# Kernel optimization log

Hardware: AMD Instinct MI355X
Metric: run time of the kernel (lower is better)

## Reference

```python
import jax, jax.numpy as jnp
import numpy as np

D = 1024
H = 16
DK = D // H


def apply_rope(x):
    # x: [B, H, T, dk]; interleaved-pair RoPE as in the torch source
    T, dim = x.shape[-2], x.shape[-1]
    inv_freq = 1.0 / (10000.0 ** (jnp.arange(0, dim, 2, dtype=x.dtype) / dim))  # [dk/2]
    pos = jnp.arange(T, dtype=x.dtype)
    sinusoid = pos[:, None] * inv_freq[None, :]  # [T, dk/2]
    sin, cos = jnp.sin(sinusoid), jnp.cos(sinusoid)
    x1, x2 = x[..., ::2], x[..., 1::2]
    rot = jnp.stack([x1 * cos - x2 * sin, x1 * sin + x2 * cos], axis=-1)
    return rot.reshape(x.shape)


def setup_inputs() -> dict:
    key = jax.random.key(0)
    k1, k2, k3, k4, k5 = jax.random.split(key, 5)
    B, T = 2, 2048
    s = 1.0 / np.sqrt(D)
    return {
        "x": jax.random.normal(k1, (B, T, D), dtype=jnp.float32),
        "W_qkv": jax.random.normal(k2, (D, 3 * D), dtype=jnp.float32) * s,
        "b_qkv": jnp.zeros((3 * D,), dtype=jnp.float32),
        "W_out": jax.random.normal(k3, (D, D), dtype=jnp.float32) * s,
        "b_out": jnp.zeros((D,), dtype=jnp.float32),
    }


def reference(x, W_qkv, b_qkv, W_out, b_out):
    B, T, C = x.shape
    qkv = x @ W_qkv + b_qkv  # [B, T, 3D]
    qkv = qkv.reshape(B, T, 3, H, DK).transpose(2, 0, 3, 1, 4)  # [3, B, H, T, dk]
    q, k, v = qkv[0], qkv[1], qkv[2]
    q, k = apply_rope(q), apply_rope(k)
    scores = jnp.einsum("bhtd,bhsd->bhts", q, k) / jnp.sqrt(jnp.asarray(DK, x.dtype))
    causal = jnp.tril(jnp.ones((T, T), dtype=bool))
    scores = jnp.where(causal, scores, jnp.asarray(-1e9, x.dtype))
    probs = jax.nn.softmax(scores, axis=-1)
    attn = jnp.einsum("bhts,bhsd->bhtd", probs, v)  # [B, H, T, dk]
    out = attn.transpose(0, 2, 1, 3).reshape(B, T, C)  # b h t d -> b t (h d)
    return out @ W_out + b_out
```

## Files before the change

### kernel.cpp

```cpp
#include <hip/hip_runtime.h>
#include <math.h>

#define DMODEL 1024
#define NHEAD  16
#define HDK    64
#define BATCH  2
#define SEQ    2048
#define MROWS  (BATCH*SEQ)
#define NQKV   (3*DMODEL)
#define LOG2_10000 13.287712379549449f
#define INV2PI 0.15915494309189535f
#define SCALE_LOG2E 0.1803368801111137f
#define M_FIX 8.0f

typedef __attribute__((ext_vector_type(8))) short bf16x8;
typedef __attribute__((ext_vector_type(4))) short s16x4;
typedef __attribute__((ext_vector_type(4))) float f32x4;
typedef __attribute__((ext_vector_type(2))) unsigned int u32x2;

__device__ __forceinline__ short f2bf(float f) {
    union { float f; unsigned u; } v; v.f = f;
    unsigned r = v.u + 0x7fffu + ((v.u >> 16) & 1u);
    return (short)(r >> 16);
}

__device__ __forceinline__ float fast_exp2(float x) {
#if __has_builtin(__builtin_amdgcn_exp2f)
    return __builtin_amdgcn_exp2f(x);
#else
    return exp2f(x);
#endif
}

__device__ __forceinline__ void gld_lds16(const short* g, short* l) {
    __builtin_amdgcn_global_load_lds(
        (const __attribute__((address_space(1))) void*)g,
        (__attribute__((address_space(3))) void*)l, 16, 0, 0);
}

__global__ __launch_bounds__(256) void prep_kernel(
    const float* __restrict__ x, const float* __restrict__ wqkv,
    const float* __restrict__ wout,
    short* __restrict__ xb, short* __restrict__ wqkv_t, short* __restrict__ wout_t)
{
    __shared__ short tile[32][33];
    const int tid = threadIdx.x;
    if (blockIdx.x < 2048) {
        const int i = (blockIdx.x * 256 + tid) * 8;
        float4 a = *(const float4*)(x + i);
        float4 b = *(const float4*)(x + i + 4);
        bf16x8 o;
        o[0] = f2bf(a.x); o[1] = f2bf(a.y); o[2] = f2bf(a.z); o[3] = f2bf(a.w);
        o[4] = f2bf(b.x); o[5] = f2bf(b.y); o[6] = f2bf(b.z); o[7] = f2bf(b.w);
        *(bf16x8*)(xb + i) = o;
        return;
    }
    const int bx = blockIdx.x - 2048;
    int nx = bx & 127;
    const int ky = bx >> 7;
    const float* in; short* out; int N;
    if (nx < 96) { in = wqkv; out = wqkv_t; N = NQKV; }
    else         { in = wout; out = wout_t; N = DMODEL; nx -= 96; }
    const int tx = tid & 31, ty = tid >> 5;
    const int n0 = nx * 32, k0 = ky * 32;
    #pragma unroll
    for (int i = 0; i < 32; i += 8)
        tile[ty + i][tx] = f2bf(in[(size_t)(k0 + ty + i) * N + n0 + tx]);
    __syncthreads();
    #pragma unroll
    for (int i = 0; i < 32; i += 8)
        out[(size_t)(n0 + ty + i) * DMODEL + k0 + tx] = tile[tx][ty + i];
}

__global__ __launch_bounds__(256) void qkv_gemm_kernel(
    const short* __restrict__ xb, const short* __restrict__ Wt,
    const float* __restrict__ bias,
    short* __restrict__ qd, short* __restrict__ kd, short* __restrict__ vtb)
{
    __shared__ __align__(16) short As[3][128 * 32];
    __shared__ __align__(16) short Bs[3][128 * 32];
    const int tid = threadIdx.x;
    const int lane = tid & 63, wave = tid >> 6;
    const int wm = wave & 1, wn = wave >> 1;
    const int l15 = lane & 15, quad = lane >> 4;
    const int n0 = blockIdx.x * 128, m0 = blockIdx.y * 128;
    const int srow = lane >> 2, sc = lane & 3;
    const int scp = sc ^ ((srow >> 1) & 3);
    const int rdx = (l15 >> 1) & 3;

    const short* gA1 = xb + (size_t)(m0 + wave * 32 + srow) * DMODEL + scp * 8;
    const short* gA2 = gA1 + (size_t)16 * DMODEL;
    const short* gB1 = Wt + (size_t)(n0 + wave * 32 + srow) * DMODEL + scp * 8;
    const short* gB2 = gB1 + (size_t)16 * DMODEL;
    const int lofsA1 = (wave * 32) * 32;
    const int lofsA2 = (wave * 32 + 16) * 32;

    f32x4 zero = {0.f, 0.f, 0.f, 0.f};
    f32x4 acc[4][4];
    #pragma unroll
    for (int i = 0; i < 4; ++i)
        #pragma unroll
        for (int j = 0; j < 4; ++j) acc[i][j] = zero;

#define QKV_COMPUTE(CUR)                                                          \
    {                                                                             \
        bf16x8 af[4], bfr[4];                                                     \
        _Pragma("unroll")                                                         \
        for (int i = 0; i < 4; ++i)                                               \
            af[i] = *(const bf16x8*)&As[CUR][(wm * 64 + i * 16 + l15) * 32 + (quad ^ rdx) * 8]; \
        _Pragma("unroll")                                                         \
        for (int j = 0; j < 4; ++j)                                               \
            bfr[j] = *(const bf16x8*)&Bs[CUR][(wn * 64 + j * 16 + l15) * 32 + (quad ^ rdx) * 8]; \
        _Pragma("unroll")                                                         \
        for (int i = 0; i < 4; ++i)                                               \
            _Pragma("unroll")                                                     \
            for (int j = 0; j < 4; ++j)                                           \
                acc[i][j] = __builtin_amdgcn_mfma_f32_16x16x32_bf16(af[i], bfr[j], acc[i][j], 0, 0, 0); \
    }

    gld_lds16(gA1, &As[0][lofsA1]);
    gld_lds16(gA2, &As[0][lofsA2]);
    gld_lds16(gB1, &Bs[0][lofsA1]);
    gld_lds16(gB2, &Bs[0][lofsA2]);
    gld_lds16(gA1 + 32, &As[1][lofsA1]);
    gld_lds16(gA2 + 32, &As[1][lofsA2]);
    gld_lds16(gB1 + 32, &Bs[1][lofsA1]);
    gld_lds16(gB2 + 32, &Bs[1][lofsA2]);

    int cur = 0, nx = 2;
    #pragma unroll 3
    for (int k = 0; k < 30; ++k) {
        const int kn = (k + 2) * 32;
        gld_lds16(gA1 + kn, &As[nx][lofsA1]);
        gld_lds16(gA2 + kn, &As[nx][lofsA2]);
        gld_lds16(gB1 + kn, &Bs[nx][lofsA1]);
        gld_lds16(gB2 + kn, &Bs[nx][lofsA2]);
        asm volatile("s_waitcnt vmcnt(8)\n\ts_barrier" ::: "memory");
        QKV_COMPUTE(cur);
        asm volatile("s_barrier" ::: "memory");
        cur = (cur == 2) ? 0 : cur + 1;
        nx  = (nx == 2) ? 0 : nx + 1;
    }
    asm volatile("s_waitcnt vmcnt(4)\n\ts_barrier" ::: "memory");
    QKV_COMPUTE(cur);
    cur = (cur == 2) ? 0 : cur + 1;
    asm volatile("s_waitcnt vmcnt(0)\n\ts_barrier" ::: "memory");
    QKV_COMPUTE(cur);
#undef QKV_COMPUTE

    const int which = n0 >> 10;
    float biasv[4], invf[4];
    int hh[4], dd[4];
    #pragma unroll
    for (int j = 0; j < 4; ++j) {
        const int n = n0 + wn * 64 + j * 16 + l15;
        biasv[j] = bias[n];
        hh[j] = (n & 1023) >> 6;
        dd[j] = n & 63;
        invf[j] = INV2PI * exp2f(-((float)(dd[j] & ~1) / 64.f) * LOG2_10000);
    }
    #pragma unroll
    for (int i = 0; i < 4; ++i) {
        const int mb = m0 + wm * 64 + i * 16 + quad * 4;
        const int b = mb >> 11, tb = mb & (SEQ - 1);
        if (which < 2) {
            #pragma unroll
            for (int j = 0; j < 4; ++j) {
                #pragma unroll
                for (int r = 0; r < 4; ++r) {
                    const int t = tb + r;
                    float val = acc[i][j][r] + biasv[j];
                    const float rev = (float)t * invf[j];
                    const float fr = rev - floorf(rev);
                    const float s = __builtin_amdgcn_sinf(fr);
                    const float c = __builtin_amdgcn_cosf(fr);
                    const float partner = __shfl_xor(val, 1);
                    val = (lane & 1) ? (partner * s + val * c) : (val * c - partner * s);
                    short* dst = (which == 0) ? qd : kd;
                    dst[((size_t)(b * NHEAD + hh[j]) * SEQ + t) * HDK + dd[j]] = f2bf(val);
                }
            }
        } else {
            #pragma unroll
            for (int j = 0; j < 4; ++j) {
                s16x4 sv;
                #pragma unroll
                for (int r = 0; r < 4; ++r)
                    sv[r] = f2bf(acc[i][j][r] + biasv[j]);
                *(s16x4*)&vtb[((size_t)(b * NHEAD + hh[j]) * HDK + dd[j]) * SEQ + tb] = sv;
            }
        }
    }
}

__global__ __launch_bounds__(512) void attn_mfma_kernel(
    const short* __restrict__ qd, const short* __restrict__ kd,
    const short* __restrict__ vt, short* __restrict__ od)
{
    __shared__ __align__(16) short Ks[2][2][64 * 32];
    __shared__ __align__(16) short Vs[2][2][64 * 32];
    __shared__ __align__(16) short Ps[8][16 * 64];
    const int tid = threadIdx.x, lane = tid & 63, w = tid >> 6;
    const int l15 = lane & 15, quad = lane >> 4;
    const int par = w >> 2;
    const int ws = w & 3;
    const int id = (int)blockIdx.x;
    const int c = id & 7, g = id >> 3;
    const int qt = 31 - (g >> 2);
    const int jj = g & 3;
    const int hb = c + 8 * jj;
    const int h = hb & 15, b = hb >> 4;
    const size_t base = ((size_t)(b * NHEAD + h)) * SEQ * HDK;
    const int stid = tid & 255;
    const int hi = tid >> 8;
    const int srow = stid >> 2, sc = stid & 3;
    const int lofs = srow * 32 + (sc ^ ((srow >> 1) & 3)) * 8;
    const int rdx = (l15 >> 1) & 3;
    const int pmask = (l15 & 3) << 2;
    f32x4 zero = {0.f, 0.f, 0.f, 0.f};

    const short* kp = kd + base + (size_t)(hi * 64 + srow) * HDK + sc * 8;
    const short* vp = vt + base + (size_t)srow * SEQ + hi * 64 + sc * 8;

    const int q0 = qt * 64;
    const int trow = q0 + ws * 16 + l15;
    bf16x8 qf[2];
    {
        const short* qrow = qd + base + (size_t)trow * HDK;
        qf[0] = *(const bf16x8*)(qrow + quad * 8);
        qf[1] = *(const bf16x8*)(qrow + 32 + quad * 8);
    }
    float l_acc = 0.f;
    f32x4 o[4];
    #pragma unroll
    for (int j = 0; j < 4; ++j) o[j] = zero;

    const int nkt = qt + 1;
    const int npair = (nkt + 1) >> 1;
    short* myPs = &Ps[w][0];

    bf16x8 rk[2], rv[2];
    rk[0] = *(const bf16x8*)kp; rk[1] = *(const bf16x8*)(kp + 32);
    rv[0] = *(const bf16x8*)vp; rv[1] = *(const bf16x8*)(vp + 32);

    for (int p = 0; p < npair; ++p) {
        __syncthreads();
        *(bf16x8*)&Ks[hi][0][lofs] = rk[0];
        *(bf16x8*)&Ks[hi][1][lofs] = rk[1];
        *(bf16x8*)&Vs[hi][0][lofs] = rv[0];
        *(bf16x8*)&Vs[hi][1][lofs] = rv[1];
        __syncthreads();
        if (p + 1 < npair) {
            const int sn = (2 * p + 2) * 64;
            const short* kn = kp + (size_t)sn * HDK;
            const short* vn = vp + sn;
            rk[0] = *(const bf16x8*)kn; rk[1] = *(const bf16x8*)(kn + 32);
            rv[0] = *(const bf16x8*)vn; rv[1] = *(const bf16x8*)(vn + 32);
        }

        const int kt = 2 * p + par;
        if (kt < nkt) {
            f32x4 sacc[4];
            __builtin_amdgcn_s_setprio(1);
            #pragma unroll
            for (int j = 0; j < 4; ++j) {
                const int ro = (j * 16 + l15) * 32 + (quad ^ rdx) * 8;
                bf16x8 kf0 = *(const bf16x8*)&Ks[par][0][ro];
                bf16x8 kf1 = *(const bf16x8*)&Ks[par][1][ro];
                sacc[j] = __builtin_amdgcn_mfma_f32_16x16x32_bf16(kf0, qf[0], zero, 0, 0, 0);
                sacc[j] = __builtin_amdgcn_mfma_f32_16x16x32_bf16(kf1, qf[1], sacc[j], 0, 0, 0);
            }
            __builtin_amdgcn_s_setprio(0);
            if (kt == nkt - 1) {
                const int s0 = kt * 64;
                #pragma unroll
                for (int j = 0; j < 4; ++j) {
                    float pv[4];
                    #pragma unroll
                    for (int r = 0; r < 4; ++r) {
                        const int scol = s0 + j * 16 + quad * 4 + r;
                        const float sv = sacc[j][r] * SCALE_LOG2E - M_FIX;
                        pv[r] = (scol > trow) ? 0.f : fast_exp2(sv);
                        l_acc += pv[r];
                    }
                    unsigned pk0, pk1;
                    asm("v_cvt_pk_bf16_f32 %0, %1, %2" : "=v"(pk0) : "v"(pv[0]), "v"(pv[1]));
                    asm("v_cvt_pk_bf16_f32 %0, %1, %2" : "=v"(pk1) : "v"(pv[2]), "v"(pv[3]));
                    const int cc = (j * 4 + quad) ^ pmask;
                    u32x2 pkv = {pk0, pk1};
                    *(u32x2*)&myPs[l15 * 64 + cc * 4] = pkv;
                }
            } else {
                #pragma unroll
                for (int j = 0; j < 4; ++j) {
                    float pv[4];
                    #pragma unroll
                    for (int r = 0; r < 4; ++r) {
                        pv[r] = fast_exp2(sacc[j][r] * SCALE_LOG2E - M_FIX);
                        l_acc += pv[r];
                    }
                    unsigned pk0, pk1;
                    asm("v_cvt_pk_bf16_f32 %0, %1, %2" : "=v"(pk0) : "v"(pv[0]), "v"(pv[1]));
                    asm("v_cvt_pk_bf16_f32 %0, %1, %2" : "=v"(pk1) : "v"(pv[2]), "v"(pv[3]));
                    const int cc = (j * 4 + quad) ^ pmask;
                    u32x2 pkv = {pk0, pk1};
                    *(u32x2*)&myPs[l15 * 64 + cc * 4] = pkv;
                }
            }
            bf16x8 pf0 = *(const bf16x8*)&myPs[l15 * 64 + ((quad * 2) ^ pmask) * 4];
            bf16x8 pf1 = *(const bf16x8*)&myPs[l15 * 64 + ((8 + quad * 2) ^ pmask) * 4];
            __builtin_amdgcn_s_setprio(1);
            #pragma unroll
            for (int j = 0; j < 4; ++j) {
                const int ro = (j * 16 + l15) * 32 + (quad ^ rdx) * 8;
                bf16x8 vf0 = *(const bf16x8*)&Vs[par][0][ro];
                bf16x8 vf1 = *(const bf16x8*)&Vs[par][1][ro];
                o[j] = __builtin_amdgcn_mfma_f32_16x16x32_bf16(pf0, vf0, o[j], 0, 0, 0);
                o[j] = __builtin_amdgcn_mfma_f32_16x16x32_bf16(pf1, vf1, o[j], 0, 0, 0);
            }
            __builtin_amdgcn_s_setprio(0);
        }
    }

    float sr = l_acc;
    sr += __shfl_xor(sr, 16);
    sr += __shfl_xor(sr, 32);

    __syncthreads();
    float* ob   = (float*)&Ks[0][0][0];
    float* lbuf = (float*)&Vs[0][0][0];
    lbuf[w * 16 + l15] = sr;
    if (par == 1) {
        const int bi = (ws * 64 + lane) * 16;
        #pragma unroll
        for (int j = 0; j < 4; ++j)
            #pragma unroll
            for (int r = 0; r < 4; ++r) ob[bi + j * 4 + r] = o[j][r];
    }
    __syncthreads();
    if (par == 0) {
        const int bi = (ws * 64 + lane) * 16;
        #pragma unroll
        for (int j = 0; j < 4; ++j)
            #pragma unroll
            for (int r = 0; r < 4; ++r) o[j][r] += ob[bi + j * 4 + r];

        #pragma unroll
        for (int r = 0; r < 4; ++r) {
            const int qq = quad * 4 + r;
            const float lt = lbuf[ws * 16 + qq] + lbuf[(ws + 4) * 16 + qq];
            const float inv = 1.f / lt;
            const int t = q0 + ws * 16 + qq;
            #pragma unroll
            for (int j = 0; j < 4; ++j)
                od[((size_t)(b * SEQ + t) * NHEAD + h) * HDK + j * 16 + l15] =
                    f2bf(o[j][r] * inv);
        }
    }
}

__global__ __launch_bounds__(256) void out_gemm_kernel(
    const short* __restrict__ Ab, const short* __restrict__ Wt,
    const float* __restrict__ bias, float* __restrict__ out)
{
    __shared__ __align__(16) short As[2][128 * 32];
    __shared__ __align__(16) short Bs[2][64 * 32];
    const int tid = threadIdx.x;
    const int lane = tid & 63, wave = tid >> 6;
    const int wm = wave & 1, wn = wave >> 1;
    const int l15 = lane & 15, quad = lane >> 4;
    const int n0 = blockIdx.x * 64, m0 = blockIdx.y * 128;
    const int srow = lane >> 2, sc = lane & 3;
    const int scp = sc ^ ((srow >> 1) & 3);
    const int rdx = (l15 >> 1) & 3;

    const short* gA1 = Ab + (size_t)(m0 + wave * 32 + srow) * DMODEL + scp * 8;
    const short* gA2 = gA1 + (size_t)16 * DMODEL;
    const short* gB1 = Wt + (size_t)(n0 + wave * 16 + srow) * DMODEL + scp * 8;
    const int lofsA1 = (wave * 32) * 32;
    const int lofsA2 = (wave * 32 + 16) * 32;
    const int lofsB  = (wave * 16) * 32;

    f32x4 zero = {0.f, 0.f, 0.f, 0.f};
    f32x4 acc[4][2];
    #pragma unroll
    for (int i = 0; i < 4; ++i)
        #pragma unroll
        for (int j = 0; j < 2; ++j) acc[i][j] = zero;

    gld_lds16(gA1, &As[0][lofsA1]);
    gld_lds16(gA2, &As[0][lofsA2]);
    gld_lds16(gB1, &Bs[0][lofsB]);
    __syncthreads();

    for (int k = 0; k < DMODEL / 32; ++k) {
        const int cur = k & 1;
        if (k + 1 < DMODEL / 32) {
            const int kn = (k + 1) * 32;
            gld_lds16(gA1 + kn, &As[cur ^ 1][lofsA1]);
            gld_lds16(gA2 + kn, &As[cur ^ 1][lofsA2]);
            gld_lds16(gB1 + kn, &Bs[cur ^ 1][lofsB]);
        }
        bf16x8 af[4], bfr[2];
        #pragma unroll
        for (int i = 0; i < 4; ++i)
            af[i] = *(const bf16x8*)&As[cur][(wm * 64 + i * 16 + l15) * 32 + (quad ^ rdx) * 8];
        #pragma unroll
        for (int j = 0; j < 2; ++j)
            bfr[j] = *(const bf16x8*)&Bs[cur][(wn * 32 + j * 16 + l15) * 32 + (quad ^ rdx) * 8];
        #pragma unroll
        for (int i = 0; i < 4; ++i)
            #pragma unroll
            for (int j = 0; j < 2; ++j)
                acc[i][j] = __builtin_amdgcn_mfma_f32_16x16x32_bf16(af[i], bfr[j], acc[i][j], 0, 0, 0);
        __syncthreads();
    }

    #pragma unroll
    for (int j = 0; j < 2; ++j) {
        const int n = n0 + wn * 32 + j * 16 + l15;
        const float bv = bias[n];
        #pragma unroll
        for (int i = 0; i < 4; ++i)
            #pragma unroll
            for (int r = 0; r < 4; ++r) {
                const int m = m0 + wm * 64 + i * 16 + quad * 4 + r;
                out[(size_t)m * DMODEL + n] = acc[i][j][r] + bv;
            }
    }
}

extern "C" void kernel_launch(void* const* d_in, const int* in_sizes, int n_in,
                              void* d_out, int out_size, void* d_ws, size_t ws_size,
                              hipStream_t stream) {
    const float* x    = (const float*)d_in[0];
    const float* Wqkv = (const float*)d_in[1];
    const float* bqkv = (const float*)d_in[2];
    const float* Wout = (const float*)d_in[3];
    const float* bout = (const float*)d_in[4];
    float* out = (float*)d_out;

    short* ws = (short*)d_ws;
    short* xb     = ws;
    short* wqkv_t = xb + (size_t)4 * 1024 * 1024;
    short* wout_t = wqkv_t + (size_t)3 * 1024 * 1024;
    short* qd     = wout_t + (size_t)1024 * 1024;
    short* kd     = qd + (size_t)4 * 1024 * 1024;
    short* vtb    = kd + (size_t)4 * 1024 * 1024;
    short* attn   = vtb + (size_t)4 * 1024 * 1024;

    prep_kernel<<<2048 + 4096, 256, 0, stream>>>(x, Wqkv, Wout, xb, wqkv_t, wout_t);

    qkv_gemm_kernel<<<dim3(NQKV / 128, MROWS / 128), 256, 0, stream>>>(
        xb, wqkv_t, bqkv, qd, kd, vtb);

    attn_mfma_kernel<<<1024, 512, 0, stream>>>(qd, kd, vtb, attn);

    out_gemm_kernel<<<dim3(DMODEL / 64, MROWS / 128), 256, 0, stream>>>(
        attn, wout_t, bout, out);
}
```

Before: 186.7 us.

## Precompute RoPE cos/sin table, vectorize weight transpose, drop attention setprio

```diff
diff --git a/kernel.cpp b/kernel.cpp
--- a/kernel.cpp
+++ b/kernel.cpp
@@ -41,9 +41,10 @@
 __global__ __launch_bounds__(256) void prep_kernel(
     const float* __restrict__ x, const float* __restrict__ wqkv,
     const float* __restrict__ wout,
-    short* __restrict__ xb, short* __restrict__ wqkv_t, short* __restrict__ wout_t)
+    short* __restrict__ xb, short* __restrict__ wqkv_t, short* __restrict__ wout_t,
+    float2* __restrict__ rope)
 {
-    __shared__ short tile[32][33];
+    __shared__ __align__(16) short tile[32][36];
     const int tid = threadIdx.x;
     if (blockIdx.x < 2048) {
         const int i = (blockIdx.x * 256 + tid) * 8;
@@ -55,26 +56,44 @@
         *(bf16x8*)(xb + i) = o;
         return;
     }
+    if (blockIdx.x >= 2048 + 4096) {
+        const int idx = (blockIdx.x - 6144) * 256 + tid;
+        const int t = idx >> 5, f = idx & 31;
+        const float invf = INV2PI * exp2f(-((float)f / 32.f) * LOG2_10000);
+        const float rev = (float)t * invf;
+        const float fr = rev - floorf(rev);
+        float2 cs;
+        cs.x = __builtin_amdgcn_cosf(fr);
+        cs.y = __builtin_amdgcn_sinf(fr);
+        rope[idx] = cs;
+        return;
+    }
     const int bx = blockIdx.x - 2048;
     int nx = bx & 127;
     const int ky = bx >> 7;
     const float* in; short* out; int N;
     if (nx < 96) { in = wqkv; out = wqkv_t; N = NQKV; }
     else         { in = wout; out = wout_t; N = DMODEL; nx -= 96; }
-    const int tx = tid & 31, ty = tid >> 5;
     const int n0 = nx * 32, k0 = ky * 32;
-    #pragma unroll
-    for (int i = 0; i < 32; i += 8)
-        tile[ty + i][tx] = f2bf(in[(size_t)(k0 + ty + i) * N + n0 + tx]);
+    {
+        const int kr = tid >> 3, nc4 = tid & 7;
+        float4 v = *(const float4*)&in[(size_t)(k0 + kr) * N + n0 + nc4 * 4];
+        tile[nc4 * 4 + 0][kr] = f2bf(v.x);
+        tile[nc4 * 4 + 1][kr] = f2bf(v.y);
+        tile[nc4 * 4 + 2][kr] = f2bf(v.z);
+        tile[nc4 * 4 + 3][kr] = f2bf(v.w);
+    }
     __syncthreads();
-    #pragma unroll
-    for (int i = 0; i < 32; i += 8)
-        out[(size_t)(n0 + ty + i) * DMODEL + k0 + tx] = tile[tx][ty + i];
+    {
+        const int nr = tid >> 3, kc4 = tid & 7;
+        *(s16x4*)&out[(size_t)(n0 + nr) * DMODEL + k0 + kc4 * 4] =
+            *(const s16x4*)&tile[nr][kc4 * 4];
+    }
 }
 
 __global__ __launch_bounds__(256) void qkv_gemm_kernel(
     const short* __restrict__ xb, const short* __restrict__ Wt,
-    const float* __restrict__ bias,
+    const float* __restrict__ bias, const float2* __restrict__ rope,
     short* __restrict__ qd, short* __restrict__ kd, short* __restrict__ vtb)
 {
     __shared__ __align__(16) short As[3][128 * 32];
@@ -149,7 +168,7 @@
 #undef QKV_COMPUTE
 
     const int which = n0 >> 10;
-    float biasv[4], invf[4];
+    float biasv[4];
     int hh[4], dd[4];
     #pragma unroll
     for (int j = 0; j < 4; ++j) {
@@ -157,7 +176,6 @@
         biasv[j] = bias[n];
         hh[j] = (n & 1023) >> 6;
         dd[j] = n & 63;
-        invf[j] = INV2PI * exp2f(-((float)(dd[j] & ~1) / 64.f) * LOG2_10000);
     }
     #pragma unroll
     for (int i = 0; i < 4; ++i) {
@@ -166,16 +184,15 @@
         if (which < 2) {
             #pragma unroll
             for (int j = 0; j < 4; ++j) {
+                const int fj = dd[j] >> 1;
                 #pragma unroll
                 for (int r = 0; r < 4; ++r) {
                     const int t = tb + r;
                     float val = acc[i][j][r] + biasv[j];
-                    const float rev = (float)t * invf[j];
-                    const float fr = rev - floorf(rev);
-                    const float s = __builtin_amdgcn_sinf(fr);
-                    const float c = __builtin_amdgcn_cosf(fr);
+                    const float2 cs = rope[t * 32 + fj];
                     const float partner = __shfl_xor(val, 1);
-                    val = (lane & 1) ? (partner * s + val * c) : (val * c - partner * s);
+                    val = (lane & 1) ? (partner * cs.y + val * cs.x)
+                                     : (val * cs.x - partner * cs.y);
                     short* dst = (which == 0) ? qd : kd;
                     dst[((size_t)(b * NHEAD + hh[j]) * SEQ + t) * HDK + dd[j]] = f2bf(val);
                 }
@@ -261,7 +278,6 @@
         const int kt = 2 * p + par;
         if (kt < nkt) {
             f32x4 sacc[4];
-            __builtin_amdgcn_s_setprio(1);
             #pragma unroll
             for (int j = 0; j < 4; ++j) {
                 const int ro = (j * 16 + l15) * 32 + (quad ^ rdx) * 8;
@@ -270,7 +286,6 @@
                 sacc[j] = __builtin_amdgcn_mfma_f32_16x16x32_bf16(kf0, qf[0], zero, 0, 0, 0);
                 sacc[j] = __builtin_amdgcn_mfma_f32_16x16x32_bf16(kf1, qf[1], sacc[j], 0, 0, 0);
             }
-            __builtin_amdgcn_s_setprio(0);
             if (kt == nkt - 1) {
                 const int s0 = kt * 64;
                 #pragma unroll
@@ -309,7 +324,6 @@
             }
             bf16x8 pf0 = *(const bf16x8*)&myPs[l15 * 64 + ((quad * 2) ^ pmask) * 4];
             bf16x8 pf1 = *(const bf16x8*)&myPs[l15 * 64 + ((8 + quad * 2) ^ pmask) * 4];
-            __builtin_amdgcn_s_setprio(1);
             #pragma unroll
             for (int j = 0; j < 4; ++j) {
                 const int ro = (j * 16 + l15) * 32 + (quad ^ rdx) * 8;
@@ -318,7 +332,6 @@
                 o[j] = __builtin_amdgcn_mfma_f32_16x16x32_bf16(pf0, vf0, o[j], 0, 0, 0);
                 o[j] = __builtin_amdgcn_mfma_f32_16x16x32_bf16(pf1, vf1, o[j], 0, 0, 0);
             }
-            __builtin_amdgcn_s_setprio(0);
         }
     }
 
@@ -448,11 +461,13 @@
     short* kd     = qd + (size_t)4 * 1024 * 1024;
     short* vtb    = kd + (size_t)4 * 1024 * 1024;
     short* attn   = vtb + (size_t)4 * 1024 * 1024;
-
-    prep_kernel<<<2048 + 4096, 256, 0, stream>>>(x, Wqkv, Wout, xb, wqkv_t, wout_t);
+    float2* rope  = (float2*)(attn + (size_t)4 * 1024 * 1024);
+
+    prep_kernel<<<2048 + 4096 + 256, 256, 0, stream>>>(
+        x, Wqkv, Wout, xb, wqkv_t, wout_t, rope);
 
     qkv_gemm_kernel<<<dim3(NQKV / 128, MROWS / 128), 256, 0, stream>>>(
-        xb, wqkv_t, bqkv, qd, kd, vtb);
+        xb, wqkv_t, bqkv, rope, qd, kd, vtb);
 
     attn_mfma_kernel<<<1024, 512, 0, stream>>>(qd, kd, vtb, attn);
 
```

Result: no change. 185.3 us (-0.8%).
